# Performance work log

Hardware: AMD Instinct MI355X
Metric: run time of the kernel (lower is better)

The kernel has to match this reference:

```python
import jax, jax.numpy as jnp
import numpy as np

B, T, F, U = 64, 1024, 128, 256  # batch, time, input features, LSTM units
LN_EPS = 1e-3  # keras LayerNormalization default epsilon


def _lstm(x, W, Uw, b):
    """Keras-style LSTM, return_sequences. x:[B,T,Fin], W:[Fin,4U], Uw:[U,4U], b:[4U].
    Gate order i, f, g(cell), o as in Keras."""
    zx = jnp.einsum('btf,fg->btg', x, W) + b  # precompute input projection [B,T,4U]

    def step(carry, z_t):
        h, c = carry
        z = z_t + h @ Uw
        i, f, g, o = jnp.split(z, 4, axis=-1)
        c = jax.nn.sigmoid(f) * c + jax.nn.sigmoid(i) * jnp.tanh(g)
        h = jax.nn.sigmoid(o) * jnp.tanh(c)
        return (h, c), h

    h0 = jnp.zeros((x.shape[0], Uw.shape[0]), x.dtype)
    _, hs = jax.lax.scan(step, (h0, h0), jnp.swapaxes(zx, 0, 1))  # [T,B,U]
    return jnp.swapaxes(hs, 0, 1)  # [B,T,U]


def _bilstm(x, Wf, Uf, bf, Wb, Ub, bb):
    fwd = _lstm(x, Wf, Uf, bf)
    bwd = _lstm(x[:, ::-1], Wb, Ub, bb)[:, ::-1]  # go_backwards + re-reverse
    return jnp.concatenate([fwd, bwd], axis=-1)  # merge_mode='concat'


def _layernorm(x, gamma, beta):
    mu = jnp.mean(x, axis=-1, keepdims=True)
    var = jnp.var(x, axis=-1, keepdims=True)
    return (x - mu) * jax.lax.rsqrt(var + LN_EPS) * gamma + beta


def setup_inputs() -> dict:
    key = jax.random.key(0)
    ks = jax.random.split(key, 16)
    s = 0.05
    p = {}
    p['x'] = jax.random.normal(ks[0], (B, T, F), dtype=jnp.float32)
    # layer 1 BiLSTM (input dim F)
    p['W1f'] = jax.random.normal(ks[1], (F, 4 * U), dtype=jnp.float32) * s
    p['U1f'] = jax.random.normal(ks[2], (U, 4 * U), dtype=jnp.float32) * s
    p['b1f'] = jnp.zeros((4 * U,), jnp.float32)
    p['W1b'] = jax.random.normal(ks[3], (F, 4 * U), dtype=jnp.float32) * s
    p['U1b'] = jax.random.normal(ks[4], (U, 4 * U), dtype=jnp.float32) * s
    p['b1b'] = jnp.zeros((4 * U,), jnp.float32)
    # LayerNorm over 2U features
    p['gamma'] = jnp.ones((2 * U,), jnp.float32)
    p['beta'] = jnp.zeros((2 * U,), jnp.float32)
    # layer 2 BiLSTM (input dim 2U)
    p['W2f'] = jax.random.normal(ks[5], (2 * U, 4 * U), dtype=jnp.float32) * s
    p['U2f'] = jax.random.normal(ks[6], (U, 4 * U), dtype=jnp.float32) * s
    p['b2f'] = jnp.zeros((4 * U,), jnp.float32)
    p['W2b'] = jax.random.normal(ks[7], (2 * U, 4 * U), dtype=jnp.float32) * s
    p['U2b'] = jax.random.normal(ks[8], (U, 4 * U), dtype=jnp.float32) * s
    p['b2b'] = jnp.zeros((4 * U,), jnp.float32)
    return p


def reference(x, W1f, U1f, b1f, W1b, U1b, b1b, gamma, beta,
              W2f, U2f, b2f, W2b, U2b, b2b):
    h1 = _bilstm(x, W1f, U1f, b1f, W1b, U1b, b1b)      # [B,T,2U]
    h1 = _layernorm(h1, gamma, beta)
    h2 = _bilstm(h1, W2f, U2f, b2f, W2b, U2b, b2b)     # [B,T,2U]
    return h2
```

## Files before the change

### kernel.cpp

```cpp
#include <hip/hip_runtime.h>


typedef __attribute__((ext_vector_type(8))) _Float16 half8;
typedef __attribute__((ext_vector_type(4))) float f32x4;
typedef __attribute__((ext_vector_type(4))) unsigned short ushort4v;
typedef __attribute__((ext_vector_type(4))) unsigned int uint4v;

#define LOG2E 1.4426950408889634f
#define SENTW 0xFFFFFFFFu

static __device__ __forceinline__ unsigned short f2h(float f) {
  _Float16 h = (_Float16)f;
  return __builtin_bit_cast(unsigned short, h);
}
static __device__ __forceinline__ float h2f(unsigned short u) {
  _Float16 h = __builtin_bit_cast(_Float16, u);
  return (float)h;
}
static __device__ __forceinline__ float sigf(float x) {
  return __builtin_amdgcn_rcpf(1.f + __builtin_amdgcn_exp2f(-LOG2E * x));
}
static __device__ __forceinline__ float tanhf_(float x) {
  return 1.f - 2.f * __builtin_amdgcn_rcpf(__builtin_amdgcn_exp2f((2.f * LOG2E) * x) + 1.f);
}

static __device__ __forceinline__ uint4v ld_b128_dev(const uint4v* p) {
  uint4v v;
  asm volatile("global_load_dwordx4 %0, %1, off sc0 sc1" : "=v"(v) : "v"(p));
  return v;
}
static __device__ __forceinline__ void st_b32_dev(unsigned* p, unsigned v) {
  asm volatile("global_store_dword %0, %1, off sc0 sc1" :: "v"(p), "v"(v) : "memory");
}

__global__ void k_fill(uint4v* p, unsigned n16) {
  const uint4v v = (uint4v){SENTW, SENTW, SENTW, SENTW};
  for (unsigned i = blockIdx.x * 256 + threadIdx.x; i < n16; i += gridDim.x * 256)
    p[i] = v;
}

__global__ void k_transpose(const float* __restrict__ in, unsigned short* __restrict__ out, int K) {
  int idx = blockIdx.x * 256 + threadIdx.x;
  int c = idx / K, k = idx - c * K;
  out[idx] = f2h(in[k * 1024 + c]);
}

__global__ void k_cvtx(const float* __restrict__ x, unsigned short* __restrict__ xb) {
  int i = blockIdx.x * 256 + threadIdx.x;
  int o = i * 4;
  int k = o & 127, row = o >> 7;
  int b = row & 63, t = row >> 6;
  const f32x4 v = *(const f32x4*)(x + (size_t)((b << 10) + t) * 128 + k);
  ushort4v r;
  r.x = f2h(v.x); r.y = f2h(v.y); r.z = f2h(v.z); r.w = f2h(v.w);
  *(ushort4v*)(xb + o) = r;
}

template<int K>
__global__ __launch_bounds__(256, 2) void k_zx(
    const unsigned short* __restrict__ A,
    const unsigned short* __restrict__ Wt_f, const unsigned short* __restrict__ Wt_b,
    const float* __restrict__ bias_f, const float* __restrict__ bias_b,
    unsigned short* __restrict__ out_f, unsigned short* __restrict__ out_b) {
  const int tid = threadIdx.x, w = tid >> 6, l = tid & 63;
  const int l16 = l & 15, lg = l >> 4;
  const int wm = w & 1, wn = w >> 1;
  const int rowbase = blockIdx.x * 128 + wm * 64;
  const int colbase = blockIdx.y * 128 + wn * 64;
  const unsigned short* Wt = blockIdx.z ? Wt_b : Wt_f;
  const float* bias = blockIdx.z ? bias_b : bias_f;
  unsigned short* out = blockIdx.z ? out_b : out_f;

  f32x4 acc[4][4];
#pragma unroll
  for (int nt = 0; nt < 4; nt++) {
    float bv = bias[colbase + nt * 16 + l16];
#pragma unroll
    for (int mt = 0; mt < 4; mt++) acc[mt][nt] = (f32x4){bv, bv, bv, bv};
  }

  for (int kf = 0; kf < K / 32; kf++) {
    const int ko = kf * 32 + lg * 8;
    half8 a[4], b[4];
#pragma unroll
    for (int mt = 0; mt < 4; mt++)
      a[mt] = *(const half8*)(A + (size_t)(rowbase + mt * 16 + l16) * K + ko);
#pragma unroll
    for (int nt = 0; nt < 4; nt++)
      b[nt] = *(const half8*)(Wt + (size_t)(colbase + nt * 16 + l16) * K + ko);
#pragma unroll
    for (int mt = 0; mt < 4; mt++)
#pragma unroll
      for (int nt = 0; nt < 4; nt++)
        acc[mt][nt] = __builtin_amdgcn_mfma_f32_16x16x32_f16(a[mt], b[nt], acc[mt][nt], 0, 0, 0);
  }

#pragma unroll
  for (int mt = 0; mt < 4; mt++) {
    const int rowchunk = rowbase + mt * 16;
    const int t = rowchunk >> 6;
    const int b0 = (rowchunk & 63) + lg * 4;
#pragma unroll
    for (int nt = 0; nt < 4; nt++) {
      const int c = colbase + nt * 16 + l16;
      ushort4v r;
      r.x = f2h(acc[mt][nt].x); r.y = f2h(acc[mt][nt].y);
      r.z = f2h(acc[mt][nt].z); r.w = f2h(acc[mt][nt].w);
      *(ushort4v*)(out + (((size_t)t << 10 | c) << 6) + b0) = r;
    }
  }
}

template<int LAYER>
__global__ __launch_bounds__(512, 2) void k_rec2(
    const unsigned short* __restrict__ zx_f, const unsigned short* __restrict__ zx_b,
    const unsigned short* __restrict__ Ut_f, const unsigned short* __restrict__ Ut_b,
    unsigned short* __restrict__ exch,
    float* __restrict__ out) {
  const int tid = threadIdx.x, wv = tid >> 6, l = tid & 63;
  const int l16 = l & 15, lg = l >> 4;
  const int bid = blockIdx.x;
  const int d = bid >> 3, g = (bid >> 1) & 3, half = bid & 1;
  const int b0 = g * 16;
  const int ug = half * 128 + wv * 16 + l16;

  const unsigned short* zx = d ? zx_b : zx_f;
  const unsigned short* Ut = d ? Ut_b : Ut_f;

  __shared__ unsigned short hlds[2 * 16 * 128];

  half8 B[4][8];
#pragma unroll
  for (int j = 0; j < 8; j++) {
    const int kf = (j < 4) ? (half * 4 + j) : ((half ^ 1) * 4 + (j - 4));
#pragma unroll
    for (int q = 0; q < 4; q++)
      B[q][j] = *(const half8*)(Ut + (size_t)(q * 256 + ug) * 256 + kf * 32 + lg * 8);
  }

  f32x4 c = (f32x4){0.f, 0.f, 0.f, 0.f};

  ushort4v zq[4];
  {
    const int t0 = d ? 1023 : 0;
#pragma unroll
    for (int q = 0; q < 4; q++)
      zq[q] = *(const ushort4v*)(zx + (((size_t)t0 << 10 | (q * 256 + ug)) << 6) + b0 + lg * 4);
  }

  for (int t = 0; t < 1024; t++) {
    const int tt = d ? 1023 - t : t;
    f32x4 acc[4];
#pragma unroll
    for (int q = 0; q < 4; q++)
      acc[q] = (f32x4){h2f(zq[q].x), h2f(zq[q].y), h2f(zq[q].z), h2f(zq[q].w)};

    if (t > 0) {
      const uint4v* rowp;
      if constexpr (LAYER == 1) {
        const int tp = d ? tt + 1 : tt - 1;
        rowp = (const uint4v*)(exch + ((size_t)tp * 64 + b0 + l16) * 512 + d * 256 + (half ^ 1) * 128);
      } else {
        rowp = (const uint4v*)(exch + (((((size_t)(t - 1) * 2 + d) * 4 + g) * 2 + (half ^ 1)) * 2048)
                               + (size_t)l16 * 128);
      }
      uint4v pv0 = ld_b128_dev(rowp + 0 + lg);
      uint4v pv1 = ld_b128_dev(rowp + 4 + lg);
      uint4v pv2 = ld_b128_dev(rowp + 8 + lg);
      uint4v pv3 = ld_b128_dev(rowp + 12 + lg);

      half8 ha[4];
#pragma unroll
      for (int kfo = 0; kfo < 4; kfo++) {
        const int idx = ((l16 * 128 + kfo * 32 + lg * 8) ^ ((l16 & 7) << 3)) + ((t - 1) & 1) * 2048;
        ha[kfo] = *(const half8*)&hlds[idx];
      }
#pragma unroll
      for (int kfo = 0; kfo < 4; kfo++)
#pragma unroll
        for (int q = 0; q < 4; q++)
          acc[q] = __builtin_amdgcn_mfma_f32_16x16x32_f16(ha[kfo], B[q][kfo], acc[q], 0, 0, 0);

      int tries = 0;
      while (true) {
        asm volatile("s_waitcnt vmcnt(0)" ::: "memory");
        __builtin_amdgcn_sched_barrier(0);
        bool ok = pv0.x != SENTW && pv0.y != SENTW && pv0.z != SENTW && pv0.w != SENTW &&
                  pv1.x != SENTW && pv1.y != SENTW && pv1.z != SENTW && pv1.w != SENTW &&
                  pv2.x != SENTW && pv2.y != SENTW && pv2.z != SENTW && pv2.w != SENTW &&
                  pv3.x != SENTW && pv3.y != SENTW && pv3.z != SENTW && pv3.w != SENTW;
        if (__all(ok)) break;
        if (++tries > (1 << 16)) break;
        __builtin_amdgcn_s_sleep(1);
        pv0 = ld_b128_dev(rowp + 0 + lg);
        pv1 = ld_b128_dev(rowp + 4 + lg);
        pv2 = ld_b128_dev(rowp + 8 + lg);
        pv3 = ld_b128_dev(rowp + 12 + lg);
      }
      __builtin_amdgcn_sched_barrier(0);

      half8 pa0 = __builtin_bit_cast(half8, pv0);
      half8 pa1 = __builtin_bit_cast(half8, pv1);
      half8 pa2 = __builtin_bit_cast(half8, pv2);
      half8 pa3 = __builtin_bit_cast(half8, pv3);
#pragma unroll
      for (int q = 0; q < 4; q++) acc[q] = __builtin_amdgcn_mfma_f32_16x16x32_f16(pa0, B[q][4], acc[q], 0, 0, 0);
#pragma unroll
      for (int q = 0; q < 4; q++) acc[q] = __builtin_amdgcn_mfma_f32_16x16x32_f16(pa1, B[q][5], acc[q], 0, 0, 0);
#pragma unroll
      for (int q = 0; q < 4; q++) acc[q] = __builtin_amdgcn_mfma_f32_16x16x32_f16(pa2, B[q][6], acc[q], 0, 0, 0);
#pragma unroll
      for (int q = 0; q < 4; q++) acc[q] = __builtin_amdgcn_mfma_f32_16x16x32_f16(pa3, B[q][7], acc[q], 0, 0, 0);
    }

    if (t + 1 < 1024) {
      const int tn = d ? tt - 1 : tt + 1;
#pragma unroll
      for (int q = 0; q < 4; q++)
        zq[q] = *(const ushort4v*)(zx + (((size_t)tn << 10 | (q * 256 + ug)) << 6) + b0 + lg * 4);
    }

    unsigned short hb16[4];
    float hf[4];
#pragma unroll
    for (int rr = 0; rr < 4; rr++) {
      const float zi = acc[0][rr], zf = acc[1][rr], zg = acc[2][rr], zo = acc[3][rr];
      const float cc = sigf(zf) * c[rr] + sigf(zi) * tanhf_(zg);
      c[rr] = cc;
      hf[rr] = sigf(zo) * tanhf_(cc);
      hb16[rr] = f2h(hf[rr]);
    }

    {
      unsigned prt[4];
#pragma unroll
      for (int rr = 0; rr < 4; rr++)
        prt[rr] = (unsigned)__shfl_xor((int)(unsigned)hb16[rr], 1);
      const int odd = l16 & 1;
      const int rb = odd ? 2 : 0;
#pragma unroll
      for (int k = 0; k < 2; k++) {
        const int rr = rb + k;
        const int bl = lg * 4 + rr;
        const unsigned lo = odd ? prt[rr] : (unsigned)hb16[rr];
        const unsigned hi = odd ? (unsigned)hb16[rr] : prt[rr];
        const unsigned pk = (lo & 0xffffu) | (hi << 16);
        if constexpr (LAYER == 1) {
          const size_t widx = (((size_t)tt * 64 + b0 + bl) * 512 + d * 256 + (ug & ~1)) >> 1;
          st_b32_dev((unsigned*)exch + widx, pk);
        } else {
          const size_t base = ((((size_t)t * 2 + d) * 4 + g) * 2 + half) * 2048;
          const size_t widx = (base + (size_t)bl * 128 + ((ug & ~1) - half * 128)) >> 1;
          st_b32_dev((unsigned*)exch + widx, pk);
        }
      }
    }

    if constexpr (LAYER == 2) {
#pragma unroll
      for (int rr = 0; rr < 4; rr++) {
        const int b = b0 + lg * 4 + rr;
        out[((size_t)b << 10 | tt) * 512 + d * 256 + ug] = hf[rr];
      }
    }

#pragma unroll
    for (int rr = 0; rr < 4; rr++) {
      const int bl = lg * 4 + rr;
      const int ul = wv * 16 + l16;
      const int idx = ((bl * 128 + ul) ^ ((bl & 7) << 3)) + (t & 1) * 2048;
      hlds[idx] = hb16[rr];
    }

    asm volatile("s_waitcnt lgkmcnt(0)" ::: "memory");
    __builtin_amdgcn_s_barrier();
  }
}

__global__ __launch_bounds__(256) void k_ln(
    const unsigned short* __restrict__ h1, const float* __restrict__ gamma,
    const float* __restrict__ beta, unsigned short* __restrict__ ln1) {
  const int tid = threadIdx.x, w = tid >> 6, l = tid & 63;
  const size_t row = (size_t)blockIdx.x * 4 + w;
  const unsigned short* src = h1 + row * 512 + l * 8;
  const ushort4v v0 = *(const ushort4v*)src;
  const ushort4v v1 = *(const ushort4v*)(src + 4);
  float xv[8] = {h2f(v0.x), h2f(v0.y), h2f(v0.z), h2f(v0.w),
                 h2f(v1.x), h2f(v1.y), h2f(v1.z), h2f(v1.w)};
  float sum = 0.f, ssq = 0.f;
#pragma unroll
  for (int i = 0; i < 8; i++) { sum += xv[i]; ssq += xv[i] * xv[i]; }
#pragma unroll
  for (int off = 32; off; off >>= 1) {
    sum += __shfl_xor(sum, off);
    ssq += __shfl_xor(ssq, off);
  }
  const float mu = sum * (1.f / 512.f);
  const float var = ssq * (1.f / 512.f) - mu * mu;
  const float rs = __builtin_amdgcn_rsqf(var + 1e-3f);
  const f32x4 g0 = *(const f32x4*)(gamma + l * 8);
  const f32x4 g1 = *(const f32x4*)(gamma + l * 8 + 4);
  const f32x4 e0 = *(const f32x4*)(beta + l * 8);
  const f32x4 e1 = *(const f32x4*)(beta + l * 8 + 4);
  float gg[8] = {g0.x, g0.y, g0.z, g0.w, g1.x, g1.y, g1.z, g1.w};
  float ee[8] = {e0.x, e0.y, e0.z, e0.w, e1.x, e1.y, e1.z, e1.w};
  unsigned short hh[8];
#pragma unroll
  for (int i = 0; i < 8; i++)
    hh[i] = f2h((xv[i] - mu) * rs * gg[i] + ee[i]);
  unsigned short* dst = ln1 + row * 512 + l * 8;
  *(ushort4v*)dst = (ushort4v){hh[0], hh[1], hh[2], hh[3]};
  *(ushort4v*)(dst + 4) = (ushort4v){hh[4], hh[5], hh[6], hh[7]};
}

extern "C" void kernel_launch(void* const* d_in, const int* in_sizes, int n_in,
                              void* d_out, int out_size, void* d_ws, size_t ws_size,
                              hipStream_t stream) {
  (void)in_sizes; (void)n_in; (void)out_size; (void)ws_size;
  const float* x     = (const float*)d_in[0];
  const float* W1f   = (const float*)d_in[1];
  const float* U1f   = (const float*)d_in[2];
  const float* b1f   = (const float*)d_in[3];
  const float* W1b   = (const float*)d_in[4];
  const float* U1b   = (const float*)d_in[5];
  const float* b1b   = (const float*)d_in[6];
  const float* gamma = (const float*)d_in[7];
  const float* beta  = (const float*)d_in[8];
  const float* W2f   = (const float*)d_in[9];
  const float* U2f   = (const float*)d_in[10];
  const float* b2f   = (const float*)d_in[11];
  const float* W2b   = (const float*)d_in[12];
  const float* U2b   = (const float*)d_in[13];
  const float* b2b   = (const float*)d_in[14];

  char* ws = (char*)d_ws;
  size_t ofs = 0;
  auto alloc = [&](size_t bytes) -> void* {
    void* p = ws + ofs;
    ofs += (bytes + 255) & ~(size_t)255;
    return p;
  };
  unsigned short* Wt1f  = (unsigned short*)alloc((size_t)1024*128*2);
  unsigned short* Wt1b  = (unsigned short*)alloc((size_t)1024*128*2);
  unsigned short* Ut1f  = (unsigned short*)alloc((size_t)1024*256*2);
  unsigned short* Ut1b  = (unsigned short*)alloc((size_t)1024*256*2);
  unsigned short* Ut2f  = (unsigned short*)alloc((size_t)1024*256*2);
  unsigned short* Ut2b  = (unsigned short*)alloc((size_t)1024*256*2);
  unsigned short* Wt2f  = (unsigned short*)alloc((size_t)1024*512*2);
  unsigned short* Wt2b  = (unsigned short*)alloc((size_t)1024*512*2);
  unsigned short* zxf   = (unsigned short*)alloc((size_t)1024*1024*64*2);
  unsigned short* zxb   = (unsigned short*)alloc((size_t)1024*1024*64*2);
  const size_t HH2_BYTES = (size_t)1024 * 2 * 4 * 2 * 16 * 128 * 2;
  unsigned short* hist  = (unsigned short*)alloc(HH2_BYTES);

  unsigned short* xb  = (unsigned short*)d_out;
  unsigned short* h1  = (unsigned short*)d_out;
  unsigned short* ln1 = (unsigned short*)d_out + (size_t)65536 * 512;

  k_transpose<<<1024 * 128 / 256, 256, 0, stream>>>(W1f, Wt1f, 128);
  k_transpose<<<1024 * 128 / 256, 256, 0, stream>>>(W1b, Wt1b, 128);
  k_transpose<<<1024 * 256 / 256, 256, 0, stream>>>(U1f, Ut1f, 256);
  k_transpose<<<1024 * 256 / 256, 256, 0, stream>>>(U1b, Ut1b, 256);
  k_transpose<<<1024 * 512 / 256, 256, 0, stream>>>(W2f, Wt2f, 512);
  k_transpose<<<1024 * 512 / 256, 256, 0, stream>>>(W2b, Wt2b, 512);
  k_transpose<<<1024 * 256 / 256, 256, 0, stream>>>(U2f, Ut2f, 256);
  k_transpose<<<1024 * 256 / 256, 256, 0, stream>>>(U2b, Ut2b, 256);
  k_cvtx<<<8192, 256, 0, stream>>>(x, xb);

  dim3 zgrid(512, 8, 2);
  k_zx<128><<<zgrid, 256, 0, stream>>>(xb, Wt1f, Wt1b, b1f, b1b, zxf, zxb);
  k_fill<<<2048, 256, 0, stream>>>((uint4v*)h1, 65536u * 512u / 8u);
  k_rec2<1><<<16, 512, 0, stream>>>(zxf, zxb, Ut1f, Ut1b, h1, nullptr);
  k_ln<<<65536 / 4, 256, 0, stream>>>(h1, gamma, beta, ln1);
  k_zx<512><<<zgrid, 256, 0, stream>>>(ln1, Wt2f, Wt2b, b2f, b2b, zxf, zxb);
  k_fill<<<2048, 256, 0, stream>>>((uint4v*)hist, (unsigned)(HH2_BYTES / 16));
  k_rec2<2><<<16, 512, 0, stream>>>(zxf, zxb, Ut2f, Ut2b, hist, (float*)d_out);
}
```

Before: 5.705 ms.

## Interleave two batch groups per block to hide cross-block exchange latency

Each recurrent block now handles two 16-row batch groups instead of one, and the grid shrinks from 16 to 8 blocks. Within each time step the block computes group A's gates while group B's peer-half data is in flight, and the reverse, with poll loads issued one phase ahead. The aim is to hide the global-memory handshake latency between the two half-blocks behind the other group's MFMA and activation work. The cost is twice the serial work per block, more registers and LDS, and half as many compute units in use.

```diff
diff --git a/kernel.cpp b/kernel.cpp
--- a/kernel.cpp
+++ b/kernel.cpp
@@ -25,12 +25,13 @@
 }
 
 static __device__ __forceinline__ uint4v ld_b128_dev(const uint4v* p) {
-  uint4v v;
-  asm volatile("global_load_dwordx4 %0, %1, off sc0 sc1" : "=v"(v) : "v"(p));
-  return v;
+  uint4v v; asm volatile("global_load_dwordx4 %0, %1, off sc0 sc1" : "=v"(v) : "v"(p)); return v;
 }
 static __device__ __forceinline__ void st_b32_dev(unsigned* p, unsigned v) {
   asm volatile("global_store_dword %0, %1, off sc0 sc1" :: "v"(p), "v"(v) : "memory");
+}
+static __device__ __forceinline__ bool nosent(const uint4v& v) {
+  return v.x != SENTW && v.y != SENTW && v.z != SENTW && v.w != SENTW;
 }
 
 __global__ void k_fill(uint4v* p, unsigned n16) {
@@ -112,7 +113,7 @@
 }
 
 template<int LAYER>
-__global__ __launch_bounds__(512, 2) void k_rec2(
+__global__ __launch_bounds__(512, 2) void k_rec4(
     const unsigned short* __restrict__ zx_f, const unsigned short* __restrict__ zx_b,
     const unsigned short* __restrict__ Ut_f, const unsigned short* __restrict__ Ut_b,
     unsigned short* __restrict__ exch,
@@ -120,14 +121,14 @@
   const int tid = threadIdx.x, wv = tid >> 6, l = tid & 63;
   const int l16 = l & 15, lg = l >> 4;
   const int bid = blockIdx.x;
-  const int d = bid >> 3, g = (bid >> 1) & 3, half = bid & 1;
-  const int b0 = g * 16;
+  const int d = bid >> 2, gp = (bid >> 1) & 1, half = bid & 1;
+  const int bA = gp * 32, bB = gp * 32 + 16;
   const int ug = half * 128 + wv * 16 + l16;
 
   const unsigned short* zx = d ? zx_b : zx_f;
   const unsigned short* Ut = d ? Ut_b : Ut_f;
 
-  __shared__ unsigned short hlds[2 * 16 * 128];
+  __shared__ unsigned short hlds[4 * 2048];
 
   half8 B[4][8];
 #pragma unroll
@@ -138,138 +139,244 @@
       B[q][j] = *(const half8*)(Ut + (size_t)(q * 256 + ug) * 256 + kf * 32 + lg * 8);
   }
 
-  f32x4 c = (f32x4){0.f, 0.f, 0.f, 0.f};
-
-  ushort4v zq[4];
+  f32x4 cA = (f32x4){0, 0, 0, 0}, cB = (f32x4){0, 0, 0, 0};
+
+  ushort4v zqA[4], zqB[4];
   {
     const int t0 = d ? 1023 : 0;
 #pragma unroll
     for (int q = 0; q < 4; q++)
-      zq[q] = *(const ushort4v*)(zx + (((size_t)t0 << 10 | (q * 256 + ug)) << 6) + b0 + lg * 4);
-  }
+      zqA[q] = *(const ushort4v*)(zx + (((size_t)t0 << 10 | (q * 256 + ug)) << 6) + bA + lg * 4);
+#pragma unroll
+    for (int q = 0; q < 4; q++)
+      zqB[q] = *(const ushort4v*)(zx + (((size_t)t0 << 10 | (q * 256 + ug)) << 6) + bB + lg * 4);
+  }
+
+  auto pollbase = [&](int ts, int b0v, int grp) -> const uint4v* {
+    if (LAYER == 1) {
+      const int trow = d ? 1023 - ts : ts;
+      return (const uint4v*)(exch + ((size_t)trow * 64 + b0v + l16) * 512 + d * 256 + (half ^ 1) * 128);
+    } else {
+      const int g = gp * 2 + grp;
+      return (const uint4v*)(exch + (((((size_t)ts * 2 + d) * 4 + g) * 2 + (half ^ 1)) * 2048)
+                             + (size_t)l16 * 128);
+    }
+  };
+
+  uint4v pA0, pA1, pA2, pA3, pB0, pB1, pB2, pB3;
+  pA0 = pA1 = pA2 = pA3 = (uint4v){0, 0, 0, 0};
+  pB0 = pB1 = pB2 = pB3 = (uint4v){0, 0, 0, 0};
 
   for (int t = 0; t < 1024; t++) {
     const int tt = d ? 1023 - t : t;
+
     f32x4 acc[4];
 #pragma unroll
     for (int q = 0; q < 4; q++)
-      acc[q] = (f32x4){h2f(zq[q].x), h2f(zq[q].y), h2f(zq[q].z), h2f(zq[q].w)};
+      acc[q] = (f32x4){h2f(zqA[q].x), h2f(zqA[q].y), h2f(zqA[q].z), h2f(zqA[q].w)};
 
     if (t > 0) {
-      const uint4v* rowp;
-      if constexpr (LAYER == 1) {
-        const int tp = d ? tt + 1 : tt - 1;
-        rowp = (const uint4v*)(exch + ((size_t)tp * 64 + b0 + l16) * 512 + d * 256 + (half ^ 1) * 128);
-      } else {
-        rowp = (const uint4v*)(exch + (((((size_t)(t - 1) * 2 + d) * 4 + g) * 2 + (half ^ 1)) * 2048)
-                               + (size_t)l16 * 128);
-      }
-      uint4v pv0 = ld_b128_dev(rowp + 0 + lg);
-      uint4v pv1 = ld_b128_dev(rowp + 4 + lg);
-      uint4v pv2 = ld_b128_dev(rowp + 8 + lg);
-      uint4v pv3 = ld_b128_dev(rowp + 12 + lg);
-
+      const int rb = (((t - 1) & 1) * 2 + 0) * 2048;
       half8 ha[4];
 #pragma unroll
-      for (int kfo = 0; kfo < 4; kfo++) {
-        const int idx = ((l16 * 128 + kfo * 32 + lg * 8) ^ ((l16 & 7) << 3)) + ((t - 1) & 1) * 2048;
-        ha[kfo] = *(const half8*)&hlds[idx];
-      }
+      for (int kfo = 0; kfo < 4; kfo++)
+        ha[kfo] = *(const half8*)&hlds[rb + ((l16 * 128 + kfo * 32 + lg * 8) ^ ((l16 & 7) << 3))];
 #pragma unroll
       for (int kfo = 0; kfo < 4; kfo++)
 #pragma unroll
         for (int q = 0; q < 4; q++)
           acc[q] = __builtin_amdgcn_mfma_f32_16x16x32_f16(ha[kfo], B[q][kfo], acc[q], 0, 0, 0);
 
+      const uint4v* pb = pollbase(t - 1, bA, 0);
       int tries = 0;
       while (true) {
         asm volatile("s_waitcnt vmcnt(0)" ::: "memory");
         __builtin_amdgcn_sched_barrier(0);
-        bool ok = pv0.x != SENTW && pv0.y != SENTW && pv0.z != SENTW && pv0.w != SENTW &&
-                  pv1.x != SENTW && pv1.y != SENTW && pv1.z != SENTW && pv1.w != SENTW &&
-                  pv2.x != SENTW && pv2.y != SENTW && pv2.z != SENTW && pv2.w != SENTW &&
-                  pv3.x != SENTW && pv3.y != SENTW && pv3.z != SENTW && pv3.w != SENTW;
-        if (__all(ok)) break;
+        if (__all(nosent(pA0) && nosent(pA1) && nosent(pA2) && nosent(pA3))) break;
         if (++tries > (1 << 16)) break;
         __builtin_amdgcn_s_sleep(1);
-        pv0 = ld_b128_dev(rowp + 0 + lg);
-        pv1 = ld_b128_dev(rowp + 4 + lg);
-        pv2 = ld_b128_dev(rowp + 8 + lg);
-        pv3 = ld_b128_dev(rowp + 12 + lg);
+        pA0 = ld_b128_dev(pb + 0 + lg);  pA1 = ld_b128_dev(pb + 4 + lg);
+        pA2 = ld_b128_dev(pb + 8 + lg);  pA3 = ld_b128_dev(pb + 12 + lg);
       }
       __builtin_amdgcn_sched_barrier(0);
 
-      half8 pa0 = __builtin_bit_cast(half8, pv0);
-      half8 pa1 = __builtin_bit_cast(half8, pv1);
-      half8 pa2 = __builtin_bit_cast(half8, pv2);
-      half8 pa3 = __builtin_bit_cast(half8, pv3);
-#pragma unroll
-      for (int q = 0; q < 4; q++) acc[q] = __builtin_amdgcn_mfma_f32_16x16x32_f16(pa0, B[q][4], acc[q], 0, 0, 0);
-#pragma unroll
-      for (int q = 0; q < 4; q++) acc[q] = __builtin_amdgcn_mfma_f32_16x16x32_f16(pa1, B[q][5], acc[q], 0, 0, 0);
-#pragma unroll
-      for (int q = 0; q < 4; q++) acc[q] = __builtin_amdgcn_mfma_f32_16x16x32_f16(pa2, B[q][6], acc[q], 0, 0, 0);
-#pragma unroll
-      for (int q = 0; q < 4; q++) acc[q] = __builtin_amdgcn_mfma_f32_16x16x32_f16(pa3, B[q][7], acc[q], 0, 0, 0);
-    }
-
-    if (t + 1 < 1024) {
-      const int tn = d ? tt - 1 : tt + 1;
-#pragma unroll
-      for (int q = 0; q < 4; q++)
-        zq[q] = *(const ushort4v*)(zx + (((size_t)tn << 10 | (q * 256 + ug)) << 6) + b0 + lg * 4);
-    }
-
-    unsigned short hb16[4];
-    float hf[4];
-#pragma unroll
-    for (int rr = 0; rr < 4; rr++) {
-      const float zi = acc[0][rr], zf = acc[1][rr], zg = acc[2][rr], zo = acc[3][rr];
-      const float cc = sigf(zf) * c[rr] + sigf(zi) * tanhf_(zg);
-      c[rr] = cc;
-      hf[rr] = sigf(zo) * tanhf_(cc);
-      hb16[rr] = f2h(hf[rr]);
+      {
+        const uint4v* qb = pollbase(t - 1, bB, 1);
+        pB0 = ld_b128_dev(qb + 0 + lg);  pB1 = ld_b128_dev(qb + 4 + lg);
+        pB2 = ld_b128_dev(qb + 8 + lg);  pB3 = ld_b128_dev(qb + 12 + lg);
+      }
+
+      half8 r0 = __builtin_bit_cast(half8, pA0), r1 = __builtin_bit_cast(half8, pA1);
+      half8 r2 = __builtin_bit_cast(half8, pA2), r3 = __builtin_bit_cast(half8, pA3);
+#pragma unroll
+      for (int q = 0; q < 4; q++) acc[q] = __builtin_amdgcn_mfma_f32_16x16x32_f16(r0, B[q][4], acc[q], 0, 0, 0);
+#pragma unroll
+      for (int q = 0; q < 4; q++) acc[q] = __builtin_amdgcn_mfma_f32_16x16x32_f16(r1, B[q][5], acc[q], 0, 0, 0);
+#pragma unroll
+      for (int q = 0; q < 4; q++) acc[q] = __builtin_amdgcn_mfma_f32_16x16x32_f16(r2, B[q][6], acc[q], 0, 0, 0);
+#pragma unroll
+      for (int q = 0; q < 4; q++) acc[q] = __builtin_amdgcn_mfma_f32_16x16x32_f16(r3, B[q][7], acc[q], 0, 0, 0);
     }
 
     {
+      unsigned short hb16[4];
+      float hf[4];
+#pragma unroll
+      for (int rr = 0; rr < 4; rr++) {
+        const float zi = acc[0][rr], zf = acc[1][rr], zg = acc[2][rr], zo = acc[3][rr];
+        const float cc = sigf(zf) * cA[rr] + sigf(zi) * tanhf_(zg);
+        cA[rr] = cc;
+        hf[rr] = sigf(zo) * tanhf_(cc);
+        hb16[rr] = f2h(hf[rr]);
+      }
       unsigned prt[4];
 #pragma unroll
       for (int rr = 0; rr < 4; rr++)
         prt[rr] = (unsigned)__shfl_xor((int)(unsigned)hb16[rr], 1);
       const int odd = l16 & 1;
-      const int rb = odd ? 2 : 0;
+      const int rb2 = odd ? 2 : 0;
 #pragma unroll
       for (int k = 0; k < 2; k++) {
-        const int rr = rb + k;
+        const int rr = rb2 + k;
         const int bl = lg * 4 + rr;
         const unsigned lo = odd ? prt[rr] : (unsigned)hb16[rr];
         const unsigned hi = odd ? (unsigned)hb16[rr] : prt[rr];
         const unsigned pk = (lo & 0xffffu) | (hi << 16);
         if constexpr (LAYER == 1) {
-          const size_t widx = (((size_t)tt * 64 + b0 + bl) * 512 + d * 256 + (ug & ~1)) >> 1;
+          const size_t widx = (((size_t)tt * 64 + bA + bl) * 512 + d * 256 + (ug & ~1)) >> 1;
           st_b32_dev((unsigned*)exch + widx, pk);
         } else {
-          const size_t base = ((((size_t)t * 2 + d) * 4 + g) * 2 + half) * 2048;
+          const size_t base = ((((size_t)t * 2 + d) * 4 + (gp * 2 + 0)) * 2 + half) * 2048;
           const size_t widx = (base + (size_t)bl * 128 + ((ug & ~1) - half * 128)) >> 1;
           st_b32_dev((unsigned*)exch + widx, pk);
         }
       }
-    }
-
-    if constexpr (LAYER == 2) {
+      if constexpr (LAYER == 2) {
+#pragma unroll
+        for (int rr = 0; rr < 4; rr++) {
+          const int b = bA + lg * 4 + rr;
+          out[((size_t)b << 10 | tt) * 512 + d * 256 + ug] = hf[rr];
+        }
+      }
 #pragma unroll
       for (int rr = 0; rr < 4; rr++) {
-        const int b = b0 + lg * 4 + rr;
-        out[((size_t)b << 10 | tt) * 512 + d * 256 + ug] = hf[rr];
-      }
-    }
-
-#pragma unroll
-    for (int rr = 0; rr < 4; rr++) {
-      const int bl = lg * 4 + rr;
-      const int ul = wv * 16 + l16;
-      const int idx = ((bl * 128 + ul) ^ ((bl & 7) << 3)) + (t & 1) * 2048;
-      hlds[idx] = hb16[rr];
+        const int bl = lg * 4 + rr;
+        const int ul = wv * 16 + l16;
+        const int idx = ((bl * 128 + ul) ^ ((bl & 7) << 3)) + ((t & 1) * 2 + 0) * 2048;
+        hlds[idx] = hb16[rr];
+      }
+    }
+    if (t + 1 < 1024) {
+      const int tn = d ? tt - 1 : tt + 1;
+#pragma unroll
+      for (int q = 0; q < 4; q++)
+        zqA[q] = *(const ushort4v*)(zx + (((size_t)tn << 10 | (q * 256 + ug)) << 6) + bA + lg * 4);
+    }
+
+#pragma unroll
+    for (int q = 0; q < 4; q++)
+      acc[q] = (f32x4){h2f(zqB[q].x), h2f(zqB[q].y), h2f(zqB[q].z), h2f(zqB[q].w)};
+
+    if (t > 0) {
+      const int rb = (((t - 1) & 1) * 2 + 1) * 2048;
+      half8 ha[4];
+#pragma unroll
+      for (int kfo = 0; kfo < 4; kfo++)
+        ha[kfo] = *(const half8*)&hlds[rb + ((l16 * 128 + kfo * 32 + lg * 8) ^ ((l16 & 7) << 3))];
+#pragma unroll
+      for (int kfo = 0; kfo < 4; kfo++)
+#pragma unroll
+        for (int q = 0; q < 4; q++)
+          acc[q] = __builtin_amdgcn_mfma_f32_16x16x32_f16(ha[kfo], B[q][kfo], acc[q], 0, 0, 0);
+
+      const uint4v* pb = pollbase(t - 1, bB, 1);
+      int tries = 0;
+      while (true) {
+        asm volatile("s_waitcnt vmcnt(0)" ::: "memory");
+        __builtin_amdgcn_sched_barrier(0);
+        if (__all(nosent(pB0) && nosent(pB1) && nosent(pB2) && nosent(pB3))) break;
+        if (++tries > (1 << 16)) break;
+        __builtin_amdgcn_s_sleep(1);
+        pB0 = ld_b128_dev(pb + 0 + lg);  pB1 = ld_b128_dev(pb + 4 + lg);
+        pB2 = ld_b128_dev(pb + 8 + lg);  pB3 = ld_b128_dev(pb + 12 + lg);
+      }
+      __builtin_amdgcn_sched_barrier(0);
+
+      {
+        const uint4v* qb = pollbase(t, bA, 0);
+        pA0 = ld_b128_dev(qb + 0 + lg);  pA1 = ld_b128_dev(qb + 4 + lg);
+        pA2 = ld_b128_dev(qb + 8 + lg);  pA3 = ld_b128_dev(qb + 12 + lg);
+      }
+
+      half8 r0 = __builtin_bit_cast(half8, pB0), r1 = __builtin_bit_cast(half8, pB1);
+      half8 r2 = __builtin_bit_cast(half8, pB2), r3 = __builtin_bit_cast(half8, pB3);
+#pragma unroll
+      for (int q = 0; q < 4; q++) acc[q] = __builtin_amdgcn_mfma_f32_16x16x32_f16(r0, B[q][4], acc[q], 0, 0, 0);
+#pragma unroll
+      for (int q = 0; q < 4; q++) acc[q] = __builtin_amdgcn_mfma_f32_16x16x32_f16(r1, B[q][5], acc[q], 0, 0, 0);
+#pragma unroll
+      for (int q = 0; q < 4; q++) acc[q] = __builtin_amdgcn_mfma_f32_16x16x32_f16(r2, B[q][6], acc[q], 0, 0, 0);
+#pragma unroll
+      for (int q = 0; q < 4; q++) acc[q] = __builtin_amdgcn_mfma_f32_16x16x32_f16(r3, B[q][7], acc[q], 0, 0, 0);
+    } else {
+      const uint4v* qb = pollbase(0, bA, 0);
+      pA0 = ld_b128_dev(qb + 0 + lg);  pA1 = ld_b128_dev(qb + 4 + lg);
+      pA2 = ld_b128_dev(qb + 8 + lg);  pA3 = ld_b128_dev(qb + 12 + lg);
+    }
+
+    {
+      unsigned short hb16[4];
+      float hf[4];
+#pragma unroll
+      for (int rr = 0; rr < 4; rr++) {
+        const float zi = acc[0][rr], zf = acc[1][rr], zg = acc[2][rr], zo = acc[3][rr];
+        const float cc = sigf(zf) * cB[rr] + sigf(zi) * tanhf_(zg);
+        cB[rr] = cc;
+        hf[rr] = sigf(zo) * tanhf_(cc);
+        hb16[rr] = f2h(hf[rr]);
+      }
+      unsigned prt[4];
+#pragma unroll
+      for (int rr = 0; rr < 4; rr++)
+        prt[rr] = (unsigned)__shfl_xor((int)(unsigned)hb16[rr], 1);
+      const int odd = l16 & 1;
+      const int rb2 = odd ? 2 : 0;
+#pragma unroll
+      for (int k = 0; k < 2; k++) {
+        const int rr = rb2 + k;
+        const int bl = lg * 4 + rr;
+        const unsigned lo = odd ? prt[rr] : (unsigned)hb16[rr];
+        const unsigned hi = odd ? (unsigned)hb16[rr] : prt[rr];
+        const unsigned pk = (lo & 0xffffu) | (hi << 16);
+        if constexpr (LAYER == 1) {
+          const size_t widx = (((size_t)tt * 64 + bB + bl) * 512 + d * 256 + (ug & ~1)) >> 1;
+          st_b32_dev((unsigned*)exch + widx, pk);
+        } else {
+          const size_t base = ((((size_t)t * 2 + d) * 4 + (gp * 2 + 1)) * 2 + half) * 2048;
+          const size_t widx = (base + (size_t)bl * 128 + ((ug & ~1) - half * 128)) >> 1;
+          st_b32_dev((unsigned*)exch + widx, pk);
+        }
+      }
+      if constexpr (LAYER == 2) {
+#pragma unroll
+        for (int rr = 0; rr < 4; rr++) {
+          const int b = bB + lg * 4 + rr;
+          out[((size_t)b << 10 | tt) * 512 + d * 256 + ug] = hf[rr];
+        }
+      }
+#pragma unroll
+      for (int rr = 0; rr < 4; rr++) {
+        const int bl = lg * 4 + rr;
+        const int ul = wv * 16 + l16;
+        const int idx = ((bl * 128 + ul) ^ ((bl & 7) << 3)) + ((t & 1) * 2 + 1) * 2048;
+        hlds[idx] = hb16[rr];
+      }
+    }
+    if (t + 1 < 1024) {
+      const int tn = d ? tt - 1 : tt + 1;
+#pragma unroll
+      for (int q = 0; q < 4; q++)
+        zqB[q] = *(const ushort4v*)(zx + (((size_t)tn << 10 | (q * 256 + ug)) << 6) + bB + lg * 4);
     }
 
     asm volatile("s_waitcnt lgkmcnt(0)" ::: "memory");
@@ -350,7 +457,7 @@
   unsigned short* Wt2b  = (unsigned short*)alloc((size_t)1024*512*2);
   unsigned short* zxf   = (unsigned short*)alloc((size_t)1024*1024*64*2);
   unsigned short* zxb   = (unsigned short*)alloc((size_t)1024*1024*64*2);
-  const size_t HH2_BYTES = (size_t)1024 * 2 * 4 * 2 * 16 * 128 * 2;
+  const size_t HH2_BYTES = (size_t)1024*2*4*2*16*128*2;
   unsigned short* hist  = (unsigned short*)alloc(HH2_BYTES);
 
   unsigned short* xb  = (unsigned short*)d_out;
@@ -370,9 +477,9 @@
   dim3 zgrid(512, 8, 2);
   k_zx<128><<<zgrid, 256, 0, stream>>>(xb, Wt1f, Wt1b, b1f, b1b, zxf, zxb);
   k_fill<<<2048, 256, 0, stream>>>((uint4v*)h1, 65536u * 512u / 8u);
-  k_rec2<1><<<16, 512, 0, stream>>>(zxf, zxb, Ut1f, Ut1b, h1, nullptr);
+  k_rec4<1><<<8, 512, 0, stream>>>(zxf, zxb, Ut1f, Ut1b, h1, nullptr);
   k_ln<<<65536 / 4, 256, 0, stream>>>(h1, gamma, beta, ln1);
   k_zx<512><<<zgrid, 256, 0, stream>>>(ln1, Wt2f, Wt2b, b2f, b2b, zxf, zxb);
   k_fill<<<2048, 256, 0, stream>>>((uint4v*)hist, (unsigned)(HH2_BYTES / 16));
-  k_rec2<2><<<16, 512, 0, stream>>>(zxf, zxb, Ut2f, Ut2b, hist, (float*)d_out);
-}
+  k_rec4<2><<<8, 512, 0, stream>>>(zxf, zxb, Ut2f, Ut2b, hist, (float*)d_out);
+}
```

Measured after the change: 17.69 ms. +210.1%, slower.

## Co-locate partner recurrent blocks on one XCD and poll with L2-scoped loads

Applied to the files above, without the earlier changes.

The recurrent kernel's block index is remapped so the two halves that exchange hidden state each step (bid and bid^8) are likely dispatched to the same XCD. At startup each block records its XCC id from a hardware register and reads its partner's. When both match, the per-step exchange polling uses sc0-only global loads, which stay at the shared L2 instead of going to system scope. This is meant to cut the latency of each cross-block hidden-state handoff on the serial time loop. It falls back to sc0 sc1 loads if the XCCs differ or after 64 failed polls, and it adds a small xcc-id handshake plus a fill launch at kernel start.

```diff
diff --git a/kernel.cpp b/kernel.cpp
--- a/kernel.cpp
+++ b/kernel.cpp
@@ -24,13 +24,17 @@
   return 1.f - 2.f * __builtin_amdgcn_rcpf(__builtin_amdgcn_exp2f((2.f * LOG2E) * x) + 1.f);
 }
 
-static __device__ __forceinline__ uint4v ld_b128_dev(const uint4v* p) {
+static __device__ __forceinline__ uint4v ld_b128_x(const uint4v* p, int slowv) {
   uint4v v;
-  asm volatile("global_load_dwordx4 %0, %1, off sc0 sc1" : "=v"(v) : "v"(p));
+  if (slowv) asm volatile("global_load_dwordx4 %0, %1, off sc0 sc1" : "=v"(v) : "v"(p));
+  else       asm volatile("global_load_dwordx4 %0, %1, off sc0"     : "=v"(v) : "v"(p));
   return v;
 }
 static __device__ __forceinline__ void st_b32_dev(unsigned* p, unsigned v) {
   asm volatile("global_store_dword %0, %1, off sc0 sc1" :: "v"(p), "v"(v) : "memory");
+}
+static __device__ __forceinline__ bool nosent(const uint4v& v) {
+  return v.x != SENTW && v.y != SENTW && v.z != SENTW && v.w != SENTW;
 }
 
 __global__ void k_fill(uint4v* p, unsigned n16) {
@@ -112,15 +116,16 @@
 }
 
 template<int LAYER>
-__global__ __launch_bounds__(512, 2) void k_rec2(
+__global__ __launch_bounds__(512, 2) void k_rec7(
     const unsigned short* __restrict__ zx_f, const unsigned short* __restrict__ zx_b,
     const unsigned short* __restrict__ Ut_f, const unsigned short* __restrict__ Ut_b,
     unsigned short* __restrict__ exch,
+    int* __restrict__ xcc,
     float* __restrict__ out) {
   const int tid = threadIdx.x, wv = tid >> 6, l = tid & 63;
   const int l16 = l & 15, lg = l >> 4;
   const int bid = blockIdx.x;
-  const int d = bid >> 3, g = (bid >> 1) & 3, half = bid & 1;
+  const int half = bid >> 3, d = (bid >> 2) & 1, g = bid & 3;
   const int b0 = g * 16;
   const int ug = half * 128 + wv * 16 + l16;
 
@@ -129,6 +134,20 @@
 
   __shared__ unsigned short hlds[2 * 16 * 128];
 
+  unsigned my_xcc = __builtin_amdgcn_s_getreg((3 << 11) | 20) & 0xFu;
+  if (tid == 0) st_b32_dev((unsigned*)&xcc[bid], my_xcc);
+  unsigned px = SENTW;
+  {
+    int gu = 0;
+    while (true) {
+      asm volatile("global_load_dword %0, %1, off sc0 sc1" : "=v"(px) : "v"(&xcc[bid ^ 8]));
+      asm volatile("s_waitcnt vmcnt(0)" ::: "memory");
+      if (px != SENTW || ++gu > (1 << 20)) break;
+      __builtin_amdgcn_s_sleep(1);
+    }
+  }
+  int slowv = (px == my_xcc && my_xcc < 8u) ? 0 : 1;
+
   half8 B[4][8];
 #pragma unroll
   for (int j = 0; j < 8; j++) {
@@ -138,7 +157,7 @@
       B[q][j] = *(const half8*)(Ut + (size_t)(q * 256 + ug) * 256 + kf * 32 + lg * 8);
   }
 
-  f32x4 c = (f32x4){0.f, 0.f, 0.f, 0.f};
+  f32x4 c = (f32x4){0, 0, 0, 0};
 
   ushort4v zq[4];
   {
@@ -164,10 +183,10 @@
         rowp = (const uint4v*)(exch + (((((size_t)(t - 1) * 2 + d) * 4 + g) * 2 + (half ^ 1)) * 2048)
                                + (size_t)l16 * 128);
       }
-      uint4v pv0 = ld_b128_dev(rowp + 0 + lg);
-      uint4v pv1 = ld_b128_dev(rowp + 4 + lg);
-      uint4v pv2 = ld_b128_dev(rowp + 8 + lg);
-      uint4v pv3 = ld_b128_dev(rowp + 12 + lg);
+      uint4v pv0 = ld_b128_x(rowp + 0 + lg, slowv);
+      uint4v pv1 = ld_b128_x(rowp + 4 + lg, slowv);
+      uint4v pv2 = ld_b128_x(rowp + 8 + lg, slowv);
+      uint4v pv3 = ld_b128_x(rowp + 12 + lg, slowv);
 
       half8 ha[4];
 #pragma unroll
@@ -185,17 +204,15 @@
       while (true) {
         asm volatile("s_waitcnt vmcnt(0)" ::: "memory");
         __builtin_amdgcn_sched_barrier(0);
-        bool ok = pv0.x != SENTW && pv0.y != SENTW && pv0.z != SENTW && pv0.w != SENTW &&
-                  pv1.x != SENTW && pv1.y != SENTW && pv1.z != SENTW && pv1.w != SENTW &&
-                  pv2.x != SENTW && pv2.y != SENTW && pv2.z != SENTW && pv2.w != SENTW &&
-                  pv3.x != SENTW && pv3.y != SENTW && pv3.z != SENTW && pv3.w != SENTW;
+        bool ok = nosent(pv0) && nosent(pv1) && nosent(pv2) && nosent(pv3);
         if (__all(ok)) break;
         if (++tries > (1 << 16)) break;
+        if (tries == 64) slowv = 1;
         __builtin_amdgcn_s_sleep(1);
-        pv0 = ld_b128_dev(rowp + 0 + lg);
-        pv1 = ld_b128_dev(rowp + 4 + lg);
-        pv2 = ld_b128_dev(rowp + 8 + lg);
-        pv3 = ld_b128_dev(rowp + 12 + lg);
+        pv0 = ld_b128_x(rowp + 0 + lg, slowv);
+        pv1 = ld_b128_x(rowp + 4 + lg, slowv);
+        pv2 = ld_b128_x(rowp + 8 + lg, slowv);
+        pv3 = ld_b128_x(rowp + 12 + lg, slowv);
       }
       __builtin_amdgcn_sched_barrier(0);
 
@@ -340,6 +357,8 @@
     ofs += (bytes + 255) & ~(size_t)255;
     return p;
   };
+  int* xcc1             = (int*)alloc(256);
+  int* xcc2             = (int*)alloc(256);
   unsigned short* Wt1f  = (unsigned short*)alloc((size_t)1024*128*2);
   unsigned short* Wt1b  = (unsigned short*)alloc((size_t)1024*128*2);
   unsigned short* Ut1f  = (unsigned short*)alloc((size_t)1024*256*2);
@@ -350,13 +369,14 @@
   unsigned short* Wt2b  = (unsigned short*)alloc((size_t)1024*512*2);
   unsigned short* zxf   = (unsigned short*)alloc((size_t)1024*1024*64*2);
   unsigned short* zxb   = (unsigned short*)alloc((size_t)1024*1024*64*2);
-  const size_t HH2_BYTES = (size_t)1024 * 2 * 4 * 2 * 16 * 128 * 2;
+  const size_t HH2_BYTES = (size_t)1024*2*4*2*16*128*2;
   unsigned short* hist  = (unsigned short*)alloc(HH2_BYTES);
 
   unsigned short* xb  = (unsigned short*)d_out;
   unsigned short* h1  = (unsigned short*)d_out;
   unsigned short* ln1 = (unsigned short*)d_out + (size_t)65536 * 512;
 
+  k_fill<<<1, 256, 0, stream>>>((uint4v*)xcc1, 32);
   k_transpose<<<1024 * 128 / 256, 256, 0, stream>>>(W1f, Wt1f, 128);
   k_transpose<<<1024 * 128 / 256, 256, 0, stream>>>(W1b, Wt1b, 128);
   k_transpose<<<1024 * 256 / 256, 256, 0, stream>>>(U1f, Ut1f, 256);
@@ -370,9 +390,9 @@
   dim3 zgrid(512, 8, 2);
   k_zx<128><<<zgrid, 256, 0, stream>>>(xb, Wt1f, Wt1b, b1f, b1b, zxf, zxb);
   k_fill<<<2048, 256, 0, stream>>>((uint4v*)h1, 65536u * 512u / 8u);
-  k_rec2<1><<<16, 512, 0, stream>>>(zxf, zxb, Ut1f, Ut1b, h1, nullptr);
+  k_rec7<1><<<16, 512, 0, stream>>>(zxf, zxb, Ut1f, Ut1b, h1, xcc1, nullptr);
   k_ln<<<65536 / 4, 256, 0, stream>>>(h1, gamma, beta, ln1);
   k_zx<512><<<zgrid, 256, 0, stream>>>(ln1, Wt2f, Wt2b, b2f, b2b, zxf, zxb);
   k_fill<<<2048, 256, 0, stream>>>((uint4v*)hist, (unsigned)(HH2_BYTES / 16));
-  k_rec2<2><<<16, 512, 0, stream>>>(zxf, zxb, Ut2f, Ut2b, hist, (float*)d_out);
-}
+  k_rec7<2><<<16, 512, 0, stream>>>(zxf, zxb, Ut2f, Ut2b, hist, xcc2, (float*)d_out);
+}
```

Result: slower. 6.167 ms (+8.1%).

## Add dedicated producer wave to poll peer hidden state into LDS

Applied to the files above, without the earlier changes.

Adds a ninth wavefront per block that polls the partner block's exchanged hidden-state half from global memory, waits until the sentinels are gone, and writes it into a double-buffered LDS area. The eight compute waves then read both halves from LDS instead of each issuing its own coherent global loads and spin loops. It also remaps block indices so the two halves of a direction/batch group sit in different block ranges. The goal is to take the cross-block exchange latency off the compute waves' critical path. In exchange, every step now depends on workgroup barriers matching between the producer and compute waves, and the occupancy hint drops to one block per CU.

```diff
diff --git a/kernel.cpp b/kernel.cpp
--- a/kernel.cpp
+++ b/kernel.cpp
@@ -25,12 +25,13 @@
 }
 
 static __device__ __forceinline__ uint4v ld_b128_dev(const uint4v* p) {
-  uint4v v;
-  asm volatile("global_load_dwordx4 %0, %1, off sc0 sc1" : "=v"(v) : "v"(p));
-  return v;
+  uint4v v; asm volatile("global_load_dwordx4 %0, %1, off sc0 sc1" : "=v"(v) : "v"(p)); return v;
 }
 static __device__ __forceinline__ void st_b32_dev(unsigned* p, unsigned v) {
   asm volatile("global_store_dword %0, %1, off sc0 sc1" :: "v"(p), "v"(v) : "memory");
+}
+static __device__ __forceinline__ bool nosent(const uint4v& v) {
+  return v.x != SENTW && v.y != SENTW && v.z != SENTW && v.w != SENTW;
 }
 
 __global__ void k_fill(uint4v* p, unsigned n16) {
@@ -112,7 +113,7 @@
 }
 
 template<int LAYER>
-__global__ __launch_bounds__(512, 2) void k_rec2(
+__global__ __launch_bounds__(576, 1) void k_rec8(
     const unsigned short* __restrict__ zx_f, const unsigned short* __restrict__ zx_b,
     const unsigned short* __restrict__ Ut_f, const unsigned short* __restrict__ Ut_b,
     unsigned short* __restrict__ exch,
@@ -120,14 +121,56 @@
   const int tid = threadIdx.x, wv = tid >> 6, l = tid & 63;
   const int l16 = l & 15, lg = l >> 4;
   const int bid = blockIdx.x;
-  const int d = bid >> 3, g = (bid >> 1) & 3, half = bid & 1;
+  const int half = bid >> 3, d = (bid >> 2) & 1, g = bid & 3;
   const int b0 = g * 16;
-  const int ug = half * 128 + wv * 16 + l16;
+  const int swz = (l16 & 7) << 3;
 
   const unsigned short* zx = d ? zx_b : zx_f;
   const unsigned short* Ut = d ? Ut_b : Ut_f;
 
-  __shared__ unsigned short hlds[2 * 16 * 128];
+  __shared__ unsigned short hlds[2 * 2048];
+  __shared__ unsigned short plds[2 * 2048];
+
+  if (wv == 8) {
+    for (int t = 0; t < 1024; t++) {
+      if (t < 1023) {
+        const uint4v* rowp;
+        if constexpr (LAYER == 1) {
+          const int trow = d ? 1023 - t : t;
+          rowp = (const uint4v*)(exch + ((size_t)trow * 64 + b0 + l16) * 512 + d * 256 + (half ^ 1) * 128);
+        } else {
+          rowp = (const uint4v*)(exch + (((((size_t)t * 2 + d) * 4 + g) * 2 + (half ^ 1)) * 2048)
+                                 + (size_t)l16 * 128);
+        }
+        uint4v v0 = ld_b128_dev(rowp + 0 + lg);
+        uint4v v1 = ld_b128_dev(rowp + 4 + lg);
+        uint4v v2 = ld_b128_dev(rowp + 8 + lg);
+        uint4v v3 = ld_b128_dev(rowp + 12 + lg);
+        int tries = 0;
+        while (true) {
+          asm volatile("s_waitcnt vmcnt(0)" ::: "memory");
+          __builtin_amdgcn_sched_barrier(0);
+          if (__all(nosent(v0) && nosent(v1) && nosent(v2) && nosent(v3))) break;
+          if (++tries > (1 << 16)) break;
+          v0 = ld_b128_dev(rowp + 0 + lg);
+          v1 = ld_b128_dev(rowp + 4 + lg);
+          v2 = ld_b128_dev(rowp + 8 + lg);
+          v3 = ld_b128_dev(rowp + 12 + lg);
+        }
+        __builtin_amdgcn_sched_barrier(0);
+        unsigned short* pb = plds + (t & 1) * 2048;
+        *(uint4v*)&pb[(l16 * 128 + 0 * 32 + lg * 8) ^ swz] = v0;
+        *(uint4v*)&pb[(l16 * 128 + 1 * 32 + lg * 8) ^ swz] = v1;
+        *(uint4v*)&pb[(l16 * 128 + 2 * 32 + lg * 8) ^ swz] = v2;
+        *(uint4v*)&pb[(l16 * 128 + 3 * 32 + lg * 8) ^ swz] = v3;
+      }
+      asm volatile("s_waitcnt lgkmcnt(0)" ::: "memory");
+      __builtin_amdgcn_s_barrier();
+    }
+    return;
+  }
+
+  const int ug = half * 128 + wv * 16 + l16;
 
   half8 B[4][8];
 #pragma unroll
@@ -138,7 +181,7 @@
       B[q][j] = *(const half8*)(Ut + (size_t)(q * 256 + ug) * 256 + kf * 32 + lg * 8);
   }
 
-  f32x4 c = (f32x4){0.f, 0.f, 0.f, 0.f};
+  f32x4 c = (f32x4){0, 0, 0, 0};
 
   ushort4v zq[4];
   {
@@ -156,61 +199,24 @@
       acc[q] = (f32x4){h2f(zq[q].x), h2f(zq[q].y), h2f(zq[q].z), h2f(zq[q].w)};
 
     if (t > 0) {
-      const uint4v* rowp;
-      if constexpr (LAYER == 1) {
-        const int tp = d ? tt + 1 : tt - 1;
-        rowp = (const uint4v*)(exch + ((size_t)tp * 64 + b0 + l16) * 512 + d * 256 + (half ^ 1) * 128);
-      } else {
-        rowp = (const uint4v*)(exch + (((((size_t)(t - 1) * 2 + d) * 4 + g) * 2 + (half ^ 1)) * 2048)
-                               + (size_t)l16 * 128);
-      }
-      uint4v pv0 = ld_b128_dev(rowp + 0 + lg);
-      uint4v pv1 = ld_b128_dev(rowp + 4 + lg);
-      uint4v pv2 = ld_b128_dev(rowp + 8 + lg);
-      uint4v pv3 = ld_b128_dev(rowp + 12 + lg);
-
-      half8 ha[4];
+      const int slot = ((t - 1) & 1) * 2048;
+      half8 ha[4], pa[4];
 #pragma unroll
       for (int kfo = 0; kfo < 4; kfo++) {
-        const int idx = ((l16 * 128 + kfo * 32 + lg * 8) ^ ((l16 & 7) << 3)) + ((t - 1) & 1) * 2048;
-        ha[kfo] = *(const half8*)&hlds[idx];
+        const int idx = (l16 * 128 + kfo * 32 + lg * 8) ^ swz;
+        ha[kfo] = *(const half8*)&hlds[slot + idx];
+        pa[kfo] = *(const half8*)&plds[slot + idx];
       }
 #pragma unroll
       for (int kfo = 0; kfo < 4; kfo++)
 #pragma unroll
         for (int q = 0; q < 4; q++)
           acc[q] = __builtin_amdgcn_mfma_f32_16x16x32_f16(ha[kfo], B[q][kfo], acc[q], 0, 0, 0);
-
-      int tries = 0;
-      while (true) {
-        asm volatile("s_waitcnt vmcnt(0)" ::: "memory");
-        __builtin_amdgcn_sched_barrier(0);
-        bool ok = pv0.x != SENTW && pv0.y != SENTW && pv0.z != SENTW && pv0.w != SENTW &&
-                  pv1.x != SENTW && pv1.y != SENTW && pv1.z != SENTW && pv1.w != SENTW &&
-                  pv2.x != SENTW && pv2.y != SENTW && pv2.z != SENTW && pv2.w != SENTW &&
-                  pv3.x != SENTW && pv3.y != SENTW && pv3.z != SENTW && pv3.w != SENTW;
-        if (__all(ok)) break;
-        if (++tries > (1 << 16)) break;
-        __builtin_amdgcn_s_sleep(1);
-        pv0 = ld_b128_dev(rowp + 0 + lg);
-        pv1 = ld_b128_dev(rowp + 4 + lg);
-        pv2 = ld_b128_dev(rowp + 8 + lg);
-        pv3 = ld_b128_dev(rowp + 12 + lg);
-      }
-      __builtin_amdgcn_sched_barrier(0);
-
-      half8 pa0 = __builtin_bit_cast(half8, pv0);
-      half8 pa1 = __builtin_bit_cast(half8, pv1);
-      half8 pa2 = __builtin_bit_cast(half8, pv2);
-      half8 pa3 = __builtin_bit_cast(half8, pv3);
-#pragma unroll
-      for (int q = 0; q < 4; q++) acc[q] = __builtin_amdgcn_mfma_f32_16x16x32_f16(pa0, B[q][4], acc[q], 0, 0, 0);
-#pragma unroll
-      for (int q = 0; q < 4; q++) acc[q] = __builtin_amdgcn_mfma_f32_16x16x32_f16(pa1, B[q][5], acc[q], 0, 0, 0);
-#pragma unroll
-      for (int q = 0; q < 4; q++) acc[q] = __builtin_amdgcn_mfma_f32_16x16x32_f16(pa2, B[q][6], acc[q], 0, 0, 0);
-#pragma unroll
-      for (int q = 0; q < 4; q++) acc[q] = __builtin_amdgcn_mfma_f32_16x16x32_f16(pa3, B[q][7], acc[q], 0, 0, 0);
+#pragma unroll
+      for (int kfo = 0; kfo < 4; kfo++)
+#pragma unroll
+        for (int q = 0; q < 4; q++)
+          acc[q] = __builtin_amdgcn_mfma_f32_16x16x32_f16(pa[kfo], B[q][4 + kfo], acc[q], 0, 0, 0);
     }
 
     if (t + 1 < 1024) {
@@ -350,7 +356,7 @@
   unsigned short* Wt2b  = (unsigned short*)alloc((size_t)1024*512*2);
   unsigned short* zxf   = (unsigned short*)alloc((size_t)1024*1024*64*2);
   unsigned short* zxb   = (unsigned short*)alloc((size_t)1024*1024*64*2);
-  const size_t HH2_BYTES = (size_t)1024 * 2 * 4 * 2 * 16 * 128 * 2;
+  const size_t HH2_BYTES = (size_t)1024*2*4*2*16*128*2;
   unsigned short* hist  = (unsigned short*)alloc(HH2_BYTES);
 
   unsigned short* xb  = (unsigned short*)d_out;
@@ -370,9 +376,9 @@
   dim3 zgrid(512, 8, 2);
   k_zx<128><<<zgrid, 256, 0, stream>>>(xb, Wt1f, Wt1b, b1f, b1b, zxf, zxb);
   k_fill<<<2048, 256, 0, stream>>>((uint4v*)h1, 65536u * 512u / 8u);
-  k_rec2<1><<<16, 512, 0, stream>>>(zxf, zxb, Ut1f, Ut1b, h1, nullptr);
+  k_rec8<1><<<16, 576, 0, stream>>>(zxf, zxb, Ut1f, Ut1b, h1, nullptr);
   k_ln<<<65536 / 4, 256, 0, stream>>>(h1, gamma, beta, ln1);
   k_zx<512><<<zgrid, 256, 0, stream>>>(ln1, Wt2f, Wt2b, b2f, b2b, zxf, zxb);
   k_fill<<<2048, 256, 0, stream>>>((uint4v*)hist, (unsigned)(HH2_BYTES / 16));
-  k_rec2<2><<<16, 512, 0, stream>>>(zxf, zxb, Ut2f, Ut2b, hist, (float*)d_out);
-}
+  k_rec8<2><<<16, 576, 0, stream>>>(zxf, zxb, Ut2f, Ut2b, hist, (float*)d_out);
+}
```

Result: slower. 9.656 ms (+69.2%).
